# Optimization experiments

Hardware: AMD Instinct MI355X
Metric: run time of the kernel (lower is better)

## Reference

```python
import jax, jax.numpy as jnp
import numpy as np

B, C, H, W = 2, 256, 48, 48
HIDDEN, NUM_HEADS = 512, 8
HEAD_DIM = HIDDEN // NUM_HEADS
EPS = 1e-5


def setup_inputs() -> dict:
    key = jax.random.key(0)
    ks = jax.random.split(key, 16)
    inp = {
        'modal1_feat': jax.random.normal(ks[0], (B, C, H, W), jnp.float32),
        'modal2_feat': jax.random.normal(ks[1], (B, C, H, W), jnp.float32),
    }
    s = 0.02  # weight init scale
    names = ['wq1', 'wk1', 'wv1', 'wq2', 'wk2', 'wv2']
    for i, nm in enumerate(names):
        inp[nm] = jax.random.normal(ks[2 + i], (HIDDEN, C), jnp.float32) * s
        inp['b' + nm[1:]] = jnp.zeros((HIDDEN,), jnp.float32)
    inp['wo1'] = jax.random.normal(ks[8], (C, HIDDEN), jnp.float32) * s
    inp['bo1'] = jnp.zeros((C,), jnp.float32)
    inp['wo2'] = jax.random.normal(ks[9], (C, HIDDEN), jnp.float32) * s
    inp['bo2'] = jnp.zeros((C,), jnp.float32)
    inp['ln1_g'] = jnp.ones((C,), jnp.float32)
    inp['ln1_b'] = jnp.zeros((C,), jnp.float32)
    inp['ln2_g'] = jnp.ones((C,), jnp.float32)
    inp['ln2_b'] = jnp.zeros((C,), jnp.float32)
    inp['wf'] = jax.random.normal(ks[10], (C, 2 * C), jnp.float32) * s
    inp['bf'] = jnp.zeros((C,), jnp.float32)
    inp['bn_g'] = jnp.ones((C,), jnp.float32)
    inp['bn_b'] = jnp.zeros((C,), jnp.float32)
    inp['bn_mean'] = jnp.zeros((C,), jnp.float32)
    inp['bn_var'] = jnp.ones((C,), jnp.float32)
    return inp


def _conv1x1(x, w, b):
    return jnp.einsum('bchw,oc->bohw', x, w) + b[None, :, None, None]


def _ln_channels(x, g, b):
    # LayerNorm over channel dim (x: [B,C,H,W]) applied in NHWC layout
    xc = x.transpose(0, 2, 3, 1)
    mu = xc.mean(-1, keepdims=True)
    var = ((xc - mu) ** 2).mean(-1, keepdims=True)
    y = (xc - mu) / jnp.sqrt(var + EPS) * g + b
    return y.transpose(0, 3, 1, 2)


def reference(modal1_feat, modal2_feat, wq1, bq1, wk1, bk1, wv1, bv1,
              wq2, bq2, wk2, bk2, wv2, bv2, wo1, bo1, wo2, bo2,
              ln1_g, ln1_b, ln2_g, ln2_b, wf, bf, bn_g, bn_b, bn_mean, bn_var):
    b_, c1, h1, w1 = modal1_feat.shape
    hw = h1 * w1
    scale = HEAD_DIM ** -0.5

    def as_q(t):  # [B,hidden,H,W] -> [B,h,L,d]
        return t.reshape(b_, NUM_HEADS, HEAD_DIM, hw).transpose(0, 1, 3, 2)

    def as_k(t):  # [B,h,d,L]
        return t.reshape(b_, NUM_HEADS, HEAD_DIM, hw)

    q1 = as_q(_conv1x1(modal1_feat, wq1, bq1))
    k1 = as_k(_conv1x1(modal1_feat, wk1, bk1))
    v1 = as_q(_conv1x1(modal1_feat, wv1, bv1))
    q2 = as_q(_conv1x1(modal2_feat, wq2, bq2))
    k2 = as_k(_conv1x1(modal2_feat, wk2, bk2))
    v2 = as_q(_conv1x1(modal2_feat, wv2, bv2))

    a12 = jax.nn.softmax(jnp.einsum('bhld,bhdm->bhlm', q1, k2) * scale, axis=-1)
    o1 = jnp.einsum('bhlm,bhmd->bhld', a12, v2).transpose(0, 1, 3, 2).reshape(b_, HIDDEN, h1, w1)
    a21 = jax.nn.softmax(jnp.einsum('bhld,bhdm->bhlm', q2, k1) * scale, axis=-1)
    o2 = jnp.einsum('bhlm,bhmd->bhld', a21, v1).transpose(0, 1, 3, 2).reshape(b_, HIDDEN, h1, w1)

    mod1_cross = _conv1x1(o1, wo1, bo1)
    mod2_cross = _conv1x1(o2, wo2, bo2)

    m1 = _ln_channels(modal1_feat + mod1_cross, ln1_g, ln1_b)
    m2 = _ln_channels(modal2_feat + mod2_cross, ln2_g, ln2_b)

    fused = jnp.concatenate([m1, m2], axis=1)
    f = _conv1x1(fused, wf, bf)
    # BatchNorm2d in eval mode (running stats)
    f = (f - bn_mean[None, :, None, None]) / jnp.sqrt(bn_var + EPS)[None, :, None, None]
    f = f * bn_g[None, :, None, None] + bn_b[None, :, None, None]
    return jax.nn.relu(f)
```

## Files before the change

### kernel.cpp

```cpp
#include <hip/hip_runtime.h>
#include <hip/hip_bf16.h>

#define HW_N 2304
#define EPS_F 1e-5f
#define QSCALE 0.18033688011112043f

typedef float f32x4 __attribute__((ext_vector_type(4)));
typedef short short8v __attribute__((ext_vector_type(8)));
typedef __bf16 bf16x8 __attribute__((ext_vector_type(8)));
typedef unsigned short u16;

__device__ __forceinline__ f32x4 mfma_bf16(bf16x8 a, bf16x8 b, f32x4 c) {
    return __builtin_amdgcn_mfma_f32_16x16x32_bf16(a, b, c, 0, 0, 0);
}
__device__ __forceinline__ bf16x8 ld8(const void* p) {
    return __builtin_bit_cast(bf16x8, *(const short8v*)p);
}
__device__ __forceinline__ unsigned short bfbits(float v) {
    return __builtin_bit_cast(unsigned short, __float2bfloat16(v));
}
__device__ __forceinline__ float b2f(u16 u) {
    unsigned x = (unsigned)u << 16;
    return __builtin_bit_cast(float, x);
}
__device__ __forceinline__ unsigned pack2(float lo, float hi) {
    return (unsigned)bfbits(lo) | ((unsigned)bfbits(hi) << 16);
}
__device__ __forceinline__ float max4(f32x4 v) {
    return fmaxf(fmaxf(v.x, v.y), fmaxf(v.z, v.w));
}

struct WPtrs { const float* s[9]; u16* d[9]; };

__global__ __launch_bounds__(256)
void conv_w_kernel(WPtrs p)
{
    const int j = blockIdx.z;
    const float* s = p.s[j];
    u16* d = p.d[j];
    const int i = (blockIdx.x * 256 + threadIdx.x) * 4;
    const float4 v = *(const float4*)(s + i);
    ushort4 pk;
    pk.x = bfbits(v.x); pk.y = bfbits(v.y); pk.z = bfbits(v.z); pk.w = bfbits(v.w);
    *(ushort4*)(d + i) = pk;
}

__global__ __launch_bounds__(256)
void prep_modal_kernel(const float* __restrict__ m1, const float* __restrict__ m2,
                       u16* __restrict__ t1, u16* __restrict__ t2)
{
    const int l0 = blockIdx.x * 64, c0 = blockIdx.y * 64;
    const int which = blockIdx.z >> 1, b = blockIdx.z & 1;
    const float* src = (which ? m2 : m1) + ((long long)b * 256 + c0) * HW_N + l0;
    u16* dst = (which ? t2 : t1) + ((long long)b * HW_N + l0) * 256 + c0;

    __shared__ float tile[64][65];
    const int t = threadIdx.x;
    const int r = t >> 4, cq = (t & 15) * 4;
#pragma unroll
    for (int i = 0; i < 4; ++i) {
        const int row = r + i * 16;
        const float4 v = *(const float4*)(src + (long long)row * HW_N + cq);
        tile[row][cq + 0] = v.x; tile[row][cq + 1] = v.y;
        tile[row][cq + 2] = v.z; tile[row][cq + 3] = v.w;
    }
    __syncthreads();
#pragma unroll
    for (int i = 0; i < 4; ++i) {
        const int lr = r + i * 16;
        ushort4 pk;
        pk.x = bfbits(tile[cq + 0][lr]);
        pk.y = bfbits(tile[cq + 1][lr]);
        pk.z = bfbits(tile[cq + 2][lr]);
        pk.w = bfbits(tile[cq + 3][lr]);
        *(ushort4*)(dst + (long long)lr * 256 + cq) = pk;
    }
}

struct GArgs {
    const u16* W[6];
    const float* bias[6];
    const u16* X[2];
    const u16* R[2];
    u16* outQ[2]; u16* outK[2]; u16* outV[2];
    float* outT[2];
    float* outC;
    const float *bnm, *bnv, *bng, *bnb;
};

template<int MODE>
__global__ __launch_bounds__(256)
void gemm_mfma(GArgs g)
{
    constexpr int KD = (MODE == 0) ? 256 : 512;
    constexpr int NS = KD / 32;
    const int z = blockIdx.y;
    const int j = blockIdx.z;
    const int mt_b = blockIdx.x / 18;
    const int nt_b = blockIdx.x - mt_b * 18;
    const int m0 = mt_b * 128, n0 = nt_b * 128;

    const u16* Wb = g.W[(MODE == 2) ? 0 : j];
    const u16* Xb0 = (MODE == 0) ? g.X[(j < 3) ? 0 : 1]
                                 : ((MODE == 1) ? g.X[j] : nullptr);

    __shared__ u16 Als[4096];
    __shared__ u16 Bls[4096];

    const int tid = threadIdx.x;
    const int w = tid >> 6, lane = tid & 63;
    const int l16 = lane & 15, lg = lane >> 4;

    const int ar0 = (((tid >> 6) << 4) | (tid & 15));
    const int k8 = (tid >> 4) & 3;

    short8v sa0, sa1, sb0, sb1;

    auto stage = [&](int kb) {
        const int koff = kb + k8 * 8;
        sa0 = *(const short8v*)(Wb + (long long)(m0 + ar0) * KD + koff);
        sa1 = *(const short8v*)(Wb + (long long)(m0 + ar0 + 64) * KD + koff);
        if constexpr (MODE == 0) {
            const u16* p = Xb0 + ((long long)z * HW_N + n0 + ar0) * 256 + koff;
            sb0 = *(const short8v*)p;
            sb1 = *(const short8v*)(p + 64LL * 256);
        } else if constexpr (MODE == 1) {
            const int head = kb >> 6;
            const u16* p = Xb0 + (((long long)z * 8 + head) * HW_N + n0 + ar0) * 64 + (koff & 63);
            sb0 = *(const short8v*)p;
            sb1 = *(const short8v*)(p + 64LL * 64);
        } else {
            const u16* Xb = (kb < 256) ? g.X[0] : g.X[1];
            const u16* p = Xb + ((long long)z * HW_N + n0 + ar0) * 256 + (koff & 255);
            sb0 = *(const short8v*)p;
            sb1 = *(const short8v*)(p + 64LL * 256);
        }
    };

    f32x4 acc[4][4];
#pragma unroll
    for (int a = 0; a < 4; ++a)
#pragma unroll
        for (int b = 0; b < 4; ++b) acc[a][b] = f32x4{0.f, 0.f, 0.f, 0.f};

    stage(0);
    for (int s = 0; s < NS; ++s) {
        __syncthreads();
        *(short8v*)((char*)Als + tid * 16) = sa0;
        *(short8v*)((char*)Als + tid * 16 + 4096) = sa1;
        *(short8v*)((char*)Bls + tid * 16) = sb0;
        *(short8v*)((char*)Bls + tid * 16 + 4096) = sb1;
        __syncthreads();
        if (s + 1 < NS) stage((s + 1) * 32);

        bf16x8 bfr[4];
#pragma unroll
        for (int nt = 0; nt < 4; ++nt)
            bfr[nt] = ld8((char*)Bls + ((w & 1) * 4 + nt) * 1024 + lane * 16);
#pragma unroll
        for (int mt = 0; mt < 4; ++mt) {
            const bf16x8 af = ld8((char*)Als + ((w >> 1) * 4 + mt) * 1024 + lane * 16);
#pragma unroll
            for (int nt = 0; nt < 4; ++nt)
                acc[mt][nt] = mfma_bf16(af, bfr[nt], acc[mt][nt]);
        }
    }

    const int mbase = m0 + (w >> 1) * 64 + 4 * lg;
    const int nbase = n0 + (w & 1) * 64 + l16;

    if constexpr (MODE == 0) {
        const int kind = j % 3, which = j / 3;
        const float* Bp = g.bias[j];
        if (kind < 2) {
            u16* T = (kind == 0) ? g.outQ[which] : g.outK[which];
            const float s = (kind == 0) ? QSCALE : 1.0f;
#pragma unroll
            for (int mt = 0; mt < 4; ++mt) {
                const int m = mbase + mt * 16;
                const float4 bv = *(const float4*)(Bp + m);
#pragma unroll
                for (int nt = 0; nt < 4; ++nt) {
                    const int l = nbase + nt * 16;
                    const f32x4 a = acc[mt][nt];
                    ushort4 pk;
                    pk.x = bfbits((a.x + bv.x) * s);
                    pk.y = bfbits((a.y + bv.y) * s);
                    pk.z = bfbits((a.z + bv.z) * s);
                    pk.w = bfbits((a.w + bv.w) * s);
                    *(ushort4*)(T + ((long long)(z * 8 + (m >> 6)) * HW_N + l) * 64 + (m & 63)) = pk;
                }
            }
        } else {
            u16* V = g.outV[which];
#pragma unroll
            for (int mt = 0; mt < 4; ++mt) {
                const int m = mbase + mt * 16;
                const float4 bv = *(const float4*)(Bp + m);
#pragma unroll
                for (int nt = 0; nt < 4; ++nt) {
                    const int l = nbase + nt * 16;
                    const f32x4 a = acc[mt][nt];
                    V[((long long)z * 512 + m + 0) * HW_N + l] = bfbits(a.x + bv.x);
                    V[((long long)z * 512 + m + 1) * HW_N + l] = bfbits(a.y + bv.y);
                    V[((long long)z * 512 + m + 2) * HW_N + l] = bfbits(a.z + bv.z);
                    V[((long long)z * 512 + m + 3) * HW_N + l] = bfbits(a.w + bv.w);
                }
            }
        }
    } else if constexpr (MODE == 1) {
        const float* Bp = g.bias[j];
        const u16* Rb = g.R[j];
        float* Ob = g.outT[j];
#pragma unroll
        for (int mt = 0; mt < 4; ++mt) {
            const int m = mbase + mt * 16;
            const float4 bv = *(const float4*)(Bp + m);
#pragma unroll
            for (int nt = 0; nt < 4; ++nt) {
                const int l = nbase + nt * 16;
                const long long rowoff = ((long long)z * HW_N + l) * 256 + m;
                const ushort4 rv = *(const ushort4*)(Rb + rowoff);
                const f32x4 a = acc[mt][nt];
                float4 o;
                o.x = a.x + bv.x + b2f(rv.x);
                o.y = a.y + bv.y + b2f(rv.y);
                o.z = a.z + bv.z + b2f(rv.z);
                o.w = a.w + bv.w + b2f(rv.w);
                *(float4*)(Ob + rowoff) = o;
            }
        }
    } else {
        const float* Bp = g.bias[0];
#pragma unroll
        for (int mt = 0; mt < 4; ++mt) {
            const int m = mbase + mt * 16;
            const float4 bv = *(const float4*)(Bp + m);
            const float4 mu = *(const float4*)(g.bnm + m);
            const float4 vr = *(const float4*)(g.bnv + m);
            const float4 ga = *(const float4*)(g.bng + m);
            const float4 be = *(const float4*)(g.bnb + m);
            const float sc0 = ga.x * rsqrtf(vr.x + EPS_F), sh0 = be.x - mu.x * sc0;
            const float sc1 = ga.y * rsqrtf(vr.y + EPS_F), sh1 = be.y - mu.y * sc1;
            const float sc2 = ga.z * rsqrtf(vr.z + EPS_F), sh2 = be.z - mu.z * sc2;
            const float sc3 = ga.w * rsqrtf(vr.w + EPS_F), sh3 = be.w - mu.w * sc3;
#pragma unroll
            for (int nt = 0; nt < 4; ++nt) {
                const int l = nbase + nt * 16;
                const f32x4 a = acc[mt][nt];
                float* O = g.outC + (long long)z * 256 * HW_N + l;
                O[(long long)(m + 0) * HW_N] = fmaxf((a.x + bv.x) * sc0 + sh0, 0.f);
                O[(long long)(m + 1) * HW_N] = fmaxf((a.y + bv.y) * sc1 + sh1, 0.f);
                O[(long long)(m + 2) * HW_N] = fmaxf((a.z + bv.z) * sc2 + sh2, 0.f);
                O[(long long)(m + 3) * HW_N] = fmaxf((a.w + bv.w) * sc3 + sh3, 0.f);
            }
        }
    }
}

__global__ __launch_bounds__(256)
void attn_mfma_kernel(const u16* __restrict__ qt0, const u16* __restrict__ kt0,
                      const u16* __restrict__ v0b,
                      const u16* __restrict__ qt1, const u16* __restrict__ kt1,
                      const u16* __restrict__ v1b,
                      u16* __restrict__ oat0T, u16* __restrict__ oat1T)
{
    const int flat = blockIdx.x;
    const int virt = (flat & 7) * 144 + (flat >> 3);
    const int lt = virt % 36;
    const int h = (virt / 36) & 7;
    const int zz = virt / 288;
    const int b = zz >> 1, dir = zz & 1;

    const u16* QT = dir ? qt1 : qt0;
    const u16* KT = dir ? kt0 : kt1;
    const u16* V  = dir ? v0b : v1b;

    const long long bh = (long long)(b * 8 + h);
    const u16* Qb = QT + bh * HW_N * 64;
    const u16* Kb = KT + bh * HW_N * 64;
    const u16* Vb = V + ((long long)b * 512 + h * 64) * HW_N;

    const int tid = threadIdx.x;
    const int w = tid >> 6, lane = tid & 63;
    const int l16 = lane & 15, lg = lane >> 4;
    const int l0 = lt * 64;

    __shared__ u16 Ks[2][64 * 64];
    __shared__ u16 Vs[2][64 * 64];
    __shared__ u16 Ps[4][16 * 64];

    bf16x8 qf0, qf1;
    {
        const u16* qrow = Qb + (long long)(l0 + 16 * w + l16) * 64 + 8 * lg;
        qf0 = ld8(qrow);
        qf1 = ld8(qrow + 32);
    }
    bf16x8 onesv;
    {
        short8v o;
#pragma unroll
        for (int i = 0; i < 8; ++i) o[i] = (short)0x3F80;
        onesv = __builtin_bit_cast(bf16x8, o);
    }

    f32x4 acc0 = {0.f, 0.f, 0.f, 0.f}, acc1 = acc0, acc2 = acc0, acc3 = acc0;
    f32x4 accs = acc0;
    float m_run = -1e30f;

    const int rsub = lane >> 3;
    const int csub = (lane & 7) * 8;
    const int r0 = 16 * w + rsub, r1 = r0 + 8;
    const int swz0 = (csub * 2) ^ ((r0 & 7) << 4);
    const int swz1 = (csub * 2) ^ ((r1 & 7) << 4);
    const int cb0 = (16 * lg) ^ ((l16 & 7) << 4);
    const int cb1 = (16 * lg + 64) ^ ((l16 & 7) << 4);

    short8v ka, kb2, va, vb2;
    auto stage = [&](int t) {
        const int m0 = t * 64;
        const u16* kbase = Kb + (long long)(m0 + 16 * w) * 64;
        ka  = *(const short8v*)(kbase + (long long)rsub * 64 + csub);
        kb2 = *(const short8v*)(kbase + (long long)(8 + rsub) * 64 + csub);
        const u16* vbase = Vb + (long long)(16 * w + rsub) * HW_N + m0 + csub;
        va  = *(const short8v*)(vbase);
        vb2 = *(const short8v*)(vbase + 8LL * HW_N);
    };
    auto commit = [&](int buf) {
        *(short8v*)((char*)Ks[buf] + r0 * 128 + swz0) = ka;
        *(short8v*)((char*)Ks[buf] + r1 * 128 + swz1) = kb2;
        *(short8v*)((char*)Vs[buf] + r0 * 128 + swz0) = va;
        *(short8v*)((char*)Vs[buf] + r1 * 128 + swz1) = vb2;
    };

    char* Pw = (char*)&Ps[w][0];
    const int pxor = l16 & 7;
    const int pw_hi = lg >> 1;
    const int pw_lo = 8 * (lg & 1);
    const int prow = l16 * 128;
    const int pr0 = prow + ((lg ^ pxor) << 4);
    const int pr1 = prow + (((4 + lg) ^ pxor) << 4);

    stage(0); commit(0); stage(1);
    __syncthreads();

    for (int t = 0; t < 36; ++t) {
        const int cur = t & 1;
        if (t + 1 < 36) commit(cur ^ 1);
        if (t + 2 < 36) stage(t + 2);

        const char* kb_ = (const char*)Ks[cur] + l16 * 128;
        f32x4 st0 = {0.f,0.f,0.f,0.f}, st1 = st0, st2 = st0, st3 = st0;
        __builtin_amdgcn_s_setprio(1);
        st0 = mfma_bf16(ld8(kb_ + 0 * 2048 + cb0), qf0, st0);
        st0 = mfma_bf16(ld8(kb_ + 0 * 2048 + cb1), qf1, st0);
        st1 = mfma_bf16(ld8(kb_ + 1 * 2048 + cb0), qf0, st1);
        st1 = mfma_bf16(ld8(kb_ + 1 * 2048 + cb1), qf1, st1);
        st2 = mfma_bf16(ld8(kb_ + 2 * 2048 + cb0), qf0, st2);
        st2 = mfma_bf16(ld8(kb_ + 2 * 2048 + cb1), qf1, st2);
        st3 = mfma_bf16(ld8(kb_ + 3 * 2048 + cb0), qf0, st3);
        st3 = mfma_bf16(ld8(kb_ + 3 * 2048 + cb1), qf1, st3);
        __builtin_amdgcn_s_setprio(0);

        float mx = fmaxf(fmaxf(max4(st0), max4(st1)), fmaxf(max4(st2), max4(st3)));
        mx = fmaxf(mx, __shfl_xor(mx, 16, 64));
        mx = fmaxf(mx, __shfl_xor(mx, 32, 64));
        if (!__all(mx <= m_run + 8.f)) {
            const float m_new = fmaxf(m_run, mx);
            const float alpha = exp2f(m_run - m_new);
            acc0 *= alpha; acc1 *= alpha; acc2 *= alpha; acc3 *= alpha;
            accs *= alpha;
            m_run = m_new;
        }

        f32x4 p0, p1, p2, p3;
        p0.x = exp2f(st0.x - m_run); p0.y = exp2f(st0.y - m_run);
        p0.z = exp2f(st0.z - m_run); p0.w = exp2f(st0.w - m_run);
        p1.x = exp2f(st1.x - m_run); p1.y = exp2f(st1.y - m_run);
        p1.z = exp2f(st1.z - m_run); p1.w = exp2f(st1.w - m_run);
        p2.x = exp2f(st2.x - m_run); p2.y = exp2f(st2.y - m_run);
        p2.z = exp2f(st2.z - m_run); p2.w = exp2f(st2.w - m_run);
        p3.x = exp2f(st3.x - m_run); p3.y = exp2f(st3.y - m_run);
        p3.z = exp2f(st3.z - m_run); p3.w = exp2f(st3.w - m_run);

        {
            uint2 u;
            u.x = pack2(p0.x, p0.y); u.y = pack2(p0.z, p0.w);
            *(uint2*)(Pw + prow + (((0 + pw_hi) ^ pxor) << 4) + pw_lo) = u;
            u.x = pack2(p1.x, p1.y); u.y = pack2(p1.z, p1.w);
            *(uint2*)(Pw + prow + (((2 + pw_hi) ^ pxor) << 4) + pw_lo) = u;
            u.x = pack2(p2.x, p2.y); u.y = pack2(p2.z, p2.w);
            *(uint2*)(Pw + prow + (((4 + pw_hi) ^ pxor) << 4) + pw_lo) = u;
            u.x = pack2(p3.x, p3.y); u.y = pack2(p3.z, p3.w);
            *(uint2*)(Pw + prow + (((6 + pw_hi) ^ pxor) << 4) + pw_lo) = u;
        }

        bf16x8 pf0 = ld8(Pw + pr0);
        bf16x8 pf1 = ld8(Pw + pr1);
        const char* vb_ = (const char*)Vs[cur] + l16 * 128;
        __builtin_amdgcn_s_setprio(1);
        acc0 = mfma_bf16(ld8(vb_ + 0 * 2048 + cb0), pf0, acc0);
        acc0 = mfma_bf16(ld8(vb_ + 0 * 2048 + cb1), pf1, acc0);
        acc1 = mfma_bf16(ld8(vb_ + 1 * 2048 + cb0), pf0, acc1);
        acc1 = mfma_bf16(ld8(vb_ + 1 * 2048 + cb1), pf1, acc1);
        acc2 = mfma_bf16(ld8(vb_ + 2 * 2048 + cb0), pf0, acc2);
        acc2 = mfma_bf16(ld8(vb_ + 2 * 2048 + cb1), pf1, acc2);
        acc3 = mfma_bf16(ld8(vb_ + 3 * 2048 + cb0), pf0, acc3);
        acc3 = mfma_bf16(ld8(vb_ + 3 * 2048 + cb1), pf1, acc3);
        accs = mfma_bf16(onesv, pf0, accs);
        accs = mfma_bf16(onesv, pf1, accs);
        __builtin_amdgcn_s_setprio(0);

        __syncthreads();
    }

    const float inv = 1.0f / accs.x;
    u16* obase = (dir ? oat1T : oat0T) +
                 ((long long)(b * 8 + h) * HW_N + l0 + 16 * w + l16) * 64;
#define OSTORE(T4, A) { \
    ushort4 pk; \
    pk.x = bfbits(A.x * inv); pk.y = bfbits(A.y * inv); \
    pk.z = bfbits(A.z * inv); pk.w = bfbits(A.w * inv); \
    *(ushort4*)(obase + (T4) * 16 + 4 * lg) = pk; }
    OSTORE(0, acc0) OSTORE(1, acc1) OSTORE(2, acc2) OSTORE(3, acc3)
#undef OSTORE
}

__global__ __launch_bounds__(256)
void ln_t_kernel(const float* __restrict__ mpre0T, const float* __restrict__ mpre1T,
                 const float* __restrict__ g1, const float* __restrict__ b1,
                 const float* __restrict__ g2, const float* __restrict__ b2,
                 u16* __restrict__ mln0T, u16* __restrict__ mln1T)
{
    const int l = blockIdx.x * 64 + (threadIdx.x >> 2);
    const int z = blockIdx.y, dir = blockIdx.z;
    const float* src = (dir ? mpre1T : mpre0T) + ((long long)z * HW_N + l) * 256;
    const float* gg = dir ? g2 : g1;
    const float* bb = dir ? b2 : b1;
    u16* dst = (dir ? mln1T : mln0T) + ((long long)z * HW_N + l) * 256;
    const int q = (threadIdx.x & 3) * 64;

    float4 vbuf[16];
    float sum = 0.f, sq = 0.f;
#pragma unroll
    for (int i = 0; i < 16; ++i) {
        const float4 v = *(const float4*)(src + q + i * 4);
        vbuf[i] = v;
        sum += (v.x + v.y) + (v.z + v.w);
        sq += (v.x * v.x + v.y * v.y) + (v.z * v.z + v.w * v.w);
    }
    sum += __shfl_xor(sum, 1, 64); sum += __shfl_xor(sum, 2, 64);
    sq  += __shfl_xor(sq, 1, 64);  sq  += __shfl_xor(sq, 2, 64);
    const float mean = sum * (1.f / 256.f);
    const float var = sq * (1.f / 256.f) - mean * mean;
    const float rstd = rsqrtf(var + EPS_F);
#pragma unroll
    for (int i = 0; i < 16; ++i) {
        const int c = q + i * 4;
        const float4 gv = *(const float4*)(gg + c);
        const float4 bv = *(const float4*)(bb + c);
        ushort4 pk;
        pk.x = bfbits((vbuf[i].x - mean) * rstd * gv.x + bv.x);
        pk.y = bfbits((vbuf[i].y - mean) * rstd * gv.y + bv.y);
        pk.z = bfbits((vbuf[i].z - mean) * rstd * gv.z + bv.z);
        pk.w = bfbits((vbuf[i].w - mean) * rstd * gv.w + bv.w);
        *(ushort4*)(dst + c) = pk;
    }
}

extern "C" void kernel_launch(void* const* d_in, const int* in_sizes, int n_in,
                              void* d_out, int out_size, void* d_ws, size_t ws_size,
                              hipStream_t stream)
{
    (void)in_sizes; (void)n_in; (void)out_size; (void)ws_size;

    const float* modal1 = (const float*)d_in[0];
    const float* modal2 = (const float*)d_in[1];
    const float* wqkv[6]; const float* bqkv[6];
    for (int j = 0; j < 6; ++j) {
        wqkv[j] = (const float*)d_in[2 + 2 * j];
        bqkv[j] = (const float*)d_in[3 + 2 * j];
    }
    const float* wo1 = (const float*)d_in[14];
    const float* bo1 = (const float*)d_in[15];
    const float* wo2 = (const float*)d_in[16];
    const float* bo2 = (const float*)d_in[17];
    const float* ln1_g = (const float*)d_in[18];
    const float* ln1_b = (const float*)d_in[19];
    const float* ln2_g = (const float*)d_in[20];
    const float* ln2_b = (const float*)d_in[21];
    const float* wf = (const float*)d_in[22];
    const float* bf = (const float*)d_in[23];
    const float* bn_g = (const float*)d_in[24];
    const float* bn_b = (const float*)d_in[25];
    const float* bn_mean = (const float*)d_in[26];
    const float* bn_var = (const float*)d_in[27];

    char* ws = (char*)d_ws;
    size_t off = 0;
    auto alloc = [&](size_t bytes) { char* p = ws + off; off += (bytes + 255) & ~(size_t)255; return p; };

    u16* modalT[2]; u16* wbf[9]; u16* qT[2]; u16* kT[2]; u16* vC[2];
    u16* oatT[2]; float* mpreT[2]; u16* mlnT[2];
    for (int i = 0; i < 2; ++i) modalT[i] = (u16*)alloc(2LL * HW_N * 256 * 2);
    for (int i = 0; i < 9; ++i) wbf[i] = (u16*)alloc(131072 * 2);
    for (int i = 0; i < 2; ++i) qT[i] = (u16*)alloc(2LL * 512 * HW_N * 2);
    for (int i = 0; i < 2; ++i) kT[i] = (u16*)alloc(2LL * 512 * HW_N * 2);
    for (int i = 0; i < 2; ++i) vC[i] = (u16*)alloc(2LL * 512 * HW_N * 2);
    for (int i = 0; i < 2; ++i) oatT[i] = (u16*)alloc(2LL * 512 * HW_N * 2);
    for (int i = 0; i < 2; ++i) mpreT[i] = (float*)alloc(2LL * HW_N * 256 * 4);
    for (int i = 0; i < 2; ++i) mlnT[i] = (u16*)alloc(2LL * HW_N * 256 * 2);

    WPtrs wp;
    for (int j = 0; j < 6; ++j) { wp.s[j] = wqkv[j]; wp.d[j] = wbf[j]; }
    wp.s[6] = wo1; wp.d[6] = wbf[6];
    wp.s[7] = wo2; wp.d[7] = wbf[7];
    wp.s[8] = wf;  wp.d[8] = wbf[8];
    conv_w_kernel<<<dim3(128, 1, 9), 256, 0, stream>>>(wp);
    prep_modal_kernel<<<dim3(36, 4, 4), 256, 0, stream>>>(modal1, modal2, modalT[0], modalT[1]);

    GArgs g0 = {};
    for (int j = 0; j < 6; ++j) { g0.W[j] = wbf[j]; g0.bias[j] = bqkv[j]; }
    g0.X[0] = modalT[0]; g0.X[1] = modalT[1];
    for (int i = 0; i < 2; ++i) { g0.outQ[i] = qT[i]; g0.outK[i] = kT[i]; g0.outV[i] = vC[i]; }
    gemm_mfma<0><<<dim3(72, 2, 6), 256, 0, stream>>>(g0);

    attn_mfma_kernel<<<dim3(36 * 8 * 4), 256, 0, stream>>>(
        qT[0], kT[0], vC[0], qT[1], kT[1], vC[1], oatT[0], oatT[1]);

    GArgs g1a = {};
    g1a.W[0] = wbf[6]; g1a.W[1] = wbf[7];
    g1a.bias[0] = bo1; g1a.bias[1] = bo2;
    g1a.X[0] = oatT[0]; g1a.X[1] = oatT[1];
    g1a.R[0] = modalT[0]; g1a.R[1] = modalT[1];
    g1a.outT[0] = mpreT[0]; g1a.outT[1] = mpreT[1];
    gemm_mfma<1><<<dim3(36, 2, 2), 256, 0, stream>>>(g1a);

    ln_t_kernel<<<dim3(36, 2, 2), 256, 0, stream>>>(
        mpreT[0], mpreT[1], ln1_g, ln1_b, ln2_g, ln2_b, mlnT[0], mlnT[1]);

    GArgs g2a = {};
    g2a.W[0] = wbf[8]; g2a.bias[0] = bf;
    g2a.X[0] = mlnT[0]; g2a.X[1] = mlnT[1];
    g2a.outC = (float*)d_out;
    g2a.bnm = bn_mean; g2a.bnv = bn_var; g2a.bng = bn_g; g2a.bnb = bn_b;
    gemm_mfma<2><<<dim3(36, 2, 1), 256, 0, stream>>>(g2a);
}
```

Baseline: 173.8 us.

## Switch attention to 32x32x16 MFMA with register-resident P via permlane swaps

Rewrites the flash-attention inner loop to use 32x32x16 bf16 MFMA tiles, so each wave handles 32 query rows and each block 128 rows; the grid is halved accordingly. The softmax probabilities stay in registers and are rearranged into the B-operand layout with v_permlane32_swap instead of round-tripping through a per-wave LDS buffer. The cross-lane max reduction also uses permlane32_swap rather than two shuffles. The aim is fewer LDS operations and better reuse of each K/V fragment. The cost is higher register pressure and fewer blocks in the grid, which may lower occupancy.

```diff
diff --git a/kernel.cpp b/kernel.cpp
--- a/kernel.cpp
+++ b/kernel.cpp
@@ -6,6 +6,8 @@
 #define QSCALE 0.18033688011112043f
 
 typedef float f32x4 __attribute__((ext_vector_type(4)));
+typedef float f32x16 __attribute__((ext_vector_type(16)));
+typedef unsigned u32x4 __attribute__((ext_vector_type(4)));
 typedef short short8v __attribute__((ext_vector_type(8)));
 typedef __bf16 bf16x8 __attribute__((ext_vector_type(8)));
 typedef unsigned short u16;
@@ -13,6 +15,9 @@
 __device__ __forceinline__ f32x4 mfma_bf16(bf16x8 a, bf16x8 b, f32x4 c) {
     return __builtin_amdgcn_mfma_f32_16x16x32_bf16(a, b, c, 0, 0, 0);
 }
+__device__ __forceinline__ f32x16 mfma32(bf16x8 a, bf16x8 b, f32x16 c) {
+    return __builtin_amdgcn_mfma_f32_32x32x16_bf16(a, b, c, 0, 0, 0);
+}
 __device__ __forceinline__ bf16x8 ld8(const void* p) {
     return __builtin_bit_cast(bf16x8, *(const short8v*)p);
 }
@@ -26,8 +31,11 @@
 __device__ __forceinline__ unsigned pack2(float lo, float hi) {
     return (unsigned)bfbits(lo) | ((unsigned)bfbits(hi) << 16);
 }
-__device__ __forceinline__ float max4(f32x4 v) {
-    return fmaxf(fmaxf(v.x, v.y), fmaxf(v.z, v.w));
+__device__ __forceinline__ f32x16 zero16() {
+    f32x16 z;
+#pragma unroll
+    for (int i = 0; i < 16; ++i) z[i] = 0.f;
+    return z;
 }
 
 struct WPtrs { const float* s[9]; u16* d[9]; };
@@ -266,10 +274,11 @@
                       u16* __restrict__ oat0T, u16* __restrict__ oat1T)
 {
     const int flat = blockIdx.x;
-    const int virt = (flat & 7) * 144 + (flat >> 3);
-    const int lt = virt % 36;
-    const int h = (virt / 36) & 7;
-    const int zz = virt / 288;
+    const int virt = (flat & 7) * 72 + (flat >> 3);
+    const int lt = virt % 18;
+    const int hz = virt / 18;
+    const int h = hz & 7;
+    const int zz = hz >> 3;
     const int b = zz >> 1, dir = zz & 1;
 
     const u16* QT = dir ? qt1 : qt0;
@@ -283,18 +292,17 @@
 
     const int tid = threadIdx.x;
     const int w = tid >> 6, lane = tid & 63;
-    const int l16 = lane & 15, lg = lane >> 4;
-    const int l0 = lt * 64;
+    const int l32 = lane & 31, hi = lane >> 5;
+    const int q0 = lt * 128 + w * 32;
 
     __shared__ u16 Ks[2][64 * 64];
     __shared__ u16 Vs[2][64 * 64];
-    __shared__ u16 Ps[4][16 * 64];
-
-    bf16x8 qf0, qf1;
+
+    bf16x8 qf0, qf1, qf2, qf3;
     {
-        const u16* qrow = Qb + (long long)(l0 + 16 * w + l16) * 64 + 8 * lg;
-        qf0 = ld8(qrow);
-        qf1 = ld8(qrow + 32);
+        const u16* qrow = Qb + (long long)(q0 + l32) * 64 + 8 * hi;
+        qf0 = ld8(qrow);       qf1 = ld8(qrow + 16);
+        qf2 = ld8(qrow + 32);  qf3 = ld8(qrow + 48);
     }
     bf16x8 onesv;
     {
@@ -304,8 +312,7 @@
         onesv = __builtin_bit_cast(bf16x8, o);
     }
 
-    f32x4 acc0 = {0.f, 0.f, 0.f, 0.f}, acc1 = acc0, acc2 = acc0, acc3 = acc0;
-    f32x4 accs = acc0;
+    f32x16 accA = zero16(), accB = zero16(), accs = zero16();
     float m_run = -1e30f;
 
     const int rsub = lane >> 3;
@@ -313,8 +320,6 @@
     const int r0 = 16 * w + rsub, r1 = r0 + 8;
     const int swz0 = (csub * 2) ^ ((r0 & 7) << 4);
     const int swz1 = (csub * 2) ^ ((r1 & 7) << 4);
-    const int cb0 = (16 * lg) ^ ((l16 & 7) << 4);
-    const int cb1 = (16 * lg + 64) ^ ((l16 & 7) << 4);
 
     short8v ka, kb2, va, vb2;
     auto stage = [&](int t) {
@@ -333,13 +338,9 @@
         *(short8v*)((char*)Vs[buf] + r1 * 128 + swz1) = vb2;
     };
 
-    char* Pw = (char*)&Ps[w][0];
-    const int pxor = l16 & 7;
-    const int pw_hi = lg >> 1;
-    const int pw_lo = 8 * (lg & 1);
-    const int prow = l16 * 128;
-    const int pr0 = prow + ((lg ^ pxor) << 4);
-    const int pr1 = prow + (((4 + lg) ^ pxor) << 4);
+    const int rb0 = l32 * 128;
+    const int rb1 = (l32 + 32) * 128;
+    const int cswz = ((l32 & 7) << 4);
 
     stage(0); commit(0); stage(1);
     __syncthreads();
@@ -349,81 +350,87 @@
         if (t + 1 < 36) commit(cur ^ 1);
         if (t + 2 < 36) stage(t + 2);
 
-        const char* kb_ = (const char*)Ks[cur] + l16 * 128;
-        f32x4 st0 = {0.f,0.f,0.f,0.f}, st1 = st0, st2 = st0, st3 = st0;
+        const char* kbase = (const char*)Ks[cur];
+        f32x16 s0 = zero16(), s1 = zero16();
         __builtin_amdgcn_s_setprio(1);
-        st0 = mfma_bf16(ld8(kb_ + 0 * 2048 + cb0), qf0, st0);
-        st0 = mfma_bf16(ld8(kb_ + 0 * 2048 + cb1), qf1, st0);
-        st1 = mfma_bf16(ld8(kb_ + 1 * 2048 + cb0), qf0, st1);
-        st1 = mfma_bf16(ld8(kb_ + 1 * 2048 + cb1), qf1, st1);
-        st2 = mfma_bf16(ld8(kb_ + 2 * 2048 + cb0), qf0, st2);
-        st2 = mfma_bf16(ld8(kb_ + 2 * 2048 + cb1), qf1, st2);
-        st3 = mfma_bf16(ld8(kb_ + 3 * 2048 + cb0), qf0, st3);
-        st3 = mfma_bf16(ld8(kb_ + 3 * 2048 + cb1), qf1, st3);
+#define QKSTEP(S, QF) { \
+        const int cb = (32 * (S) + 16 * hi) ^ cswz; \
+        s0 = mfma32(ld8(kbase + rb0 + cb), QF, s0); \
+        s1 = mfma32(ld8(kbase + rb1 + cb), QF, s1); }
+        QKSTEP(0, qf0) QKSTEP(1, qf1) QKSTEP(2, qf2) QKSTEP(3, qf3)
+#undef QKSTEP
         __builtin_amdgcn_s_setprio(0);
 
-        float mx = fmaxf(fmaxf(max4(st0), max4(st1)), fmaxf(max4(st2), max4(st3)));
-        mx = fmaxf(mx, __shfl_xor(mx, 16, 64));
-        mx = fmaxf(mx, __shfl_xor(mx, 32, 64));
+        f32x16 mv;
+#pragma unroll
+        for (int i = 0; i < 16; ++i) mv[i] = fmaxf(s0[i], s1[i]);
+        float ma = fmaxf(fmaxf(mv[0], mv[1]), fmaxf(mv[2], mv[3]));
+        float mb = fmaxf(fmaxf(mv[4], mv[5]), fmaxf(mv[6], mv[7]));
+        float mc = fmaxf(fmaxf(mv[8], mv[9]), fmaxf(mv[10], mv[11]));
+        float md = fmaxf(fmaxf(mv[12], mv[13]), fmaxf(mv[14], mv[15]));
+        float mx = fmaxf(fmaxf(ma, mb), fmaxf(mc, md));
+        {
+            unsigned mu = __builtin_bit_cast(unsigned, mx);
+            unsigned mv2 = mu;
+            asm("v_permlane32_swap_b32 %0, %1" : "+v"(mu), "+v"(mv2));
+            mx = fmaxf(__builtin_bit_cast(float, mu), __builtin_bit_cast(float, mv2));
+        }
+
         if (!__all(mx <= m_run + 8.f)) {
             const float m_new = fmaxf(m_run, mx);
             const float alpha = exp2f(m_run - m_new);
-            acc0 *= alpha; acc1 *= alpha; acc2 *= alpha; acc3 *= alpha;
-            accs *= alpha;
+#pragma unroll
+            for (int i = 0; i < 16; ++i) {
+                accA[i] *= alpha; accB[i] *= alpha; accs[i] *= alpha;
+            }
             m_run = m_new;
         }
 
-        f32x4 p0, p1, p2, p3;
-        p0.x = exp2f(st0.x - m_run); p0.y = exp2f(st0.y - m_run);
-        p0.z = exp2f(st0.z - m_run); p0.w = exp2f(st0.w - m_run);
-        p1.x = exp2f(st1.x - m_run); p1.y = exp2f(st1.y - m_run);
-        p1.z = exp2f(st1.z - m_run); p1.w = exp2f(st1.w - m_run);
-        p2.x = exp2f(st2.x - m_run); p2.y = exp2f(st2.y - m_run);
-        p2.z = exp2f(st2.z - m_run); p2.w = exp2f(st2.w - m_run);
-        p3.x = exp2f(st3.x - m_run); p3.y = exp2f(st3.y - m_run);
-        p3.z = exp2f(st3.z - m_run); p3.w = exp2f(st3.w - m_run);
-
-        {
-            uint2 u;
-            u.x = pack2(p0.x, p0.y); u.y = pack2(p0.z, p0.w);
-            *(uint2*)(Pw + prow + (((0 + pw_hi) ^ pxor) << 4) + pw_lo) = u;
-            u.x = pack2(p1.x, p1.y); u.y = pack2(p1.z, p1.w);
-            *(uint2*)(Pw + prow + (((2 + pw_hi) ^ pxor) << 4) + pw_lo) = u;
-            u.x = pack2(p2.x, p2.y); u.y = pack2(p2.z, p2.w);
-            *(uint2*)(Pw + prow + (((4 + pw_hi) ^ pxor) << 4) + pw_lo) = u;
-            u.x = pack2(p3.x, p3.y); u.y = pack2(p3.z, p3.w);
-            *(uint2*)(Pw + prow + (((6 + pw_hi) ^ pxor) << 4) + pw_lo) = u;
-        }
-
-        bf16x8 pf0 = ld8(Pw + pr0);
-        bf16x8 pf1 = ld8(Pw + pr1);
-        const char* vb_ = (const char*)Vs[cur] + l16 * 128;
+#pragma unroll
+        for (int i = 0; i < 16; ++i) {
+            s0[i] = exp2f(s0[i] - m_run);
+            s1[i] = exp2f(s1[i] - m_run);
+        }
+
+        const char* vbase = (const char*)Vs[cur];
         __builtin_amdgcn_s_setprio(1);
-        acc0 = mfma_bf16(ld8(vb_ + 0 * 2048 + cb0), pf0, acc0);
-        acc0 = mfma_bf16(ld8(vb_ + 0 * 2048 + cb1), pf1, acc0);
-        acc1 = mfma_bf16(ld8(vb_ + 1 * 2048 + cb0), pf0, acc1);
-        acc1 = mfma_bf16(ld8(vb_ + 1 * 2048 + cb1), pf1, acc1);
-        acc2 = mfma_bf16(ld8(vb_ + 2 * 2048 + cb0), pf0, acc2);
-        acc2 = mfma_bf16(ld8(vb_ + 2 * 2048 + cb1), pf1, acc2);
-        acc3 = mfma_bf16(ld8(vb_ + 3 * 2048 + cb0), pf0, acc3);
-        acc3 = mfma_bf16(ld8(vb_ + 3 * 2048 + cb1), pf1, acc3);
-        accs = mfma_bf16(onesv, pf0, accs);
-        accs = mfma_bf16(onesv, pf1, accs);
+#define PVSTEP(S, PT) { \
+        constexpr int qe = 2 * ((S) & 1), qo = qe + 1; \
+        unsigned a0 = pack2(PT[4 * qe + 0], PT[4 * qe + 1]); \
+        unsigned b0 = pack2(PT[4 * qe + 2], PT[4 * qe + 3]); \
+        unsigned a1 = pack2(PT[4 * qo + 0], PT[4 * qo + 1]); \
+        unsigned b1 = pack2(PT[4 * qo + 2], PT[4 * qo + 3]); \
+        asm("v_permlane32_swap_b32 %0, %1" : "+v"(a0), "+v"(a1)); \
+        asm("v_permlane32_swap_b32 %0, %1" : "+v"(b0), "+v"(b1)); \
+        u32x4 pw = {a0, b0, a1, b1}; \
+        const bf16x8 pf = __builtin_bit_cast(bf16x8, pw); \
+        const int cb = (32 * (S) + 16 * hi) ^ cswz; \
+        accA = mfma32(ld8(vbase + rb0 + cb), pf, accA); \
+        accB = mfma32(ld8(vbase + rb1 + cb), pf, accB); \
+        accs = mfma32(onesv, pf, accs); }
+        PVSTEP(0, s0) PVSTEP(1, s0) PVSTEP(2, s1) PVSTEP(3, s1)
+#undef PVSTEP
         __builtin_amdgcn_s_setprio(0);
 
         __syncthreads();
     }
 
-    const float inv = 1.0f / accs.x;
-    u16* obase = (dir ? oat1T : oat0T) +
-                 ((long long)(b * 8 + h) * HW_N + l0 + 16 * w + l16) * 64;
-#define OSTORE(T4, A) { \
-    ushort4 pk; \
-    pk.x = bfbits(A.x * inv); pk.y = bfbits(A.y * inv); \
-    pk.z = bfbits(A.z * inv); pk.w = bfbits(A.w * inv); \
-    *(ushort4*)(obase + (T4) * 16 + 4 * lg) = pk; }
-    OSTORE(0, acc0) OSTORE(1, acc1) OSTORE(2, acc2) OSTORE(3, acc3)
-#undef OSTORE
+    const float inv = 1.0f / accs[0];
+    u16* obase = (dir ? oat1T : oat0T) + (bh * HW_N + q0 + l32) * 64;
+#pragma unroll
+    for (int g = 0; g < 4; ++g) {
+        ushort4 pk;
+        pk.x = bfbits(accA[4 * g + 0] * inv);
+        pk.y = bfbits(accA[4 * g + 1] * inv);
+        pk.z = bfbits(accA[4 * g + 2] * inv);
+        pk.w = bfbits(accA[4 * g + 3] * inv);
+        *(ushort4*)(obase + 8 * g + 4 * hi) = pk;
+        pk.x = bfbits(accB[4 * g + 0] * inv);
+        pk.y = bfbits(accB[4 * g + 1] * inv);
+        pk.z = bfbits(accB[4 * g + 2] * inv);
+        pk.w = bfbits(accB[4 * g + 3] * inv);
+        *(ushort4*)(obase + 32 + 8 * g + 4 * hi) = pk;
+    }
 }
 
 __global__ __launch_bounds__(256)
@@ -525,7 +532,7 @@
     for (int i = 0; i < 2; ++i) { g0.outQ[i] = qT[i]; g0.outK[i] = kT[i]; g0.outV[i] = vC[i]; }
     gemm_mfma<0><<<dim3(72, 2, 6), 256, 0, stream>>>(g0);
 
-    attn_mfma_kernel<<<dim3(36 * 8 * 4), 256, 0, stream>>>(
+    attn_mfma_kernel<<<dim3(576), 256, 0, stream>>>(
         qT[0], kT[0], vC[0], qT[1], kT[1], vC[1], oatT[0], oatT[1]);
 
     GArgs g1a = {};
```

Result: slower. 192.3 us (+10.6%).
